# Kernel optimization log

Hardware: AMD Instinct MI355X
Metric: run time of the kernel (lower is better)

## Reference

```python
import jax, jax.numpy as jnp
import numpy as np

IN_FEATS = 512
OUT_FEATS = 512
N = 8192
M = 8192


def setup_inputs() -> dict:
    key = jax.random.key(0)
    k1, k2, k3 = jax.random.split(key, 3)
    feat_p = jax.random.normal(k1, (N, IN_FEATS), dtype=jnp.float32)
    feat_s = jax.random.normal(k2, (M, IN_FEATS), dtype=jnp.float32)
    # He (kaiming uniform) init: bound = sqrt(6 / fan_in)
    bound = float(np.sqrt(6.0 / IN_FEATS))
    weight_a = jax.random.uniform(k3, (IN_FEATS, OUT_FEATS), dtype=jnp.float32,
                                  minval=-bound, maxval=bound)
    return {"feat_p": feat_p, "feat_s": feat_s, "weight_a": weight_a}


def reference(feat_p, feat_s, weight_a):
    h_i = feat_p @ weight_a            # [N, out]
    h_j = feat_s @ weight_a            # [M, out]
    a_ij = jax.nn.relu(h_i @ h_j.T)    # [N, M]
    fro = jnp.sqrt(jnp.sum(a_ij * a_ij))
    alpha = a_ij / fro                 # global Frobenius-norm normalization
    c_i = alpha @ feat_s               # [N, in]
    return c_i
```

## Files before the change

kernel.cpp:

```cpp
#include <hip/hip_runtime.h>
#include <hip/hip_bf16.h>

#define NROWS 8192
#define DIM   512

typedef short v8s __attribute__((ext_vector_type(8)));
typedef float v4f __attribute__((ext_vector_type(4)));

#define ASM_VMCNT(n) asm volatile("s_waitcnt vmcnt(" #n ")" ::: "memory")
#define ASM_LGKM0    asm volatile("s_waitcnt lgkmcnt(0)" ::: "memory")
#define ASM_FENCE    asm volatile("" ::: "memory")
#define BAR          __builtin_amdgcn_s_barrier()

__device__ __forceinline__ short f2bf(float f) {
    union { float f; unsigned u; } v; v.f = f;
    unsigned r = (v.u + 0x7fffu + ((v.u >> 16) & 1u)) >> 16;
    return (short)r;
}

__device__ __forceinline__ void stage16(const void* g, void* l) {
    typedef __attribute__((address_space(1))) const unsigned GA;
    typedef __attribute__((address_space(3))) unsigned LA;
    __builtin_amdgcn_global_load_lds((GA*)(const unsigned*)g, (LA*)(unsigned*)l, 16, 0, 0);
}

__global__ __launch_bounds__(256) void transpose_cast_kernel(
        const float* __restrict__ in, short* __restrict__ out, int R, int C) {
    __shared__ float t[32][33];
    const int lx = threadIdx.x & 31;
    const int ly = threadIdx.x >> 5;
    const int r0 = blockIdx.x * 32;
    const int c0 = blockIdx.y * 32;
#pragma unroll
    for (int p = 0; p < 4; ++p)
        t[ly + 8 * p][lx] = in[(size_t)(r0 + ly + 8 * p) * C + c0 + lx];
    __syncthreads();
#pragma unroll
    for (int p = 0; p < 4; ++p)
        out[(size_t)(c0 + ly + 8 * p) * R + r0 + lx] = f2bf(t[lx][ly + 8 * p]);
}

__global__ __launch_bounds__(512) void gemm1_kernel(
        const float* __restrict__ Fp, const float* __restrict__ Fs,
        const short* __restrict__ WT,
        short* __restrict__ Hp, short* __restrict__ Hs) {
    const float* F = blockIdx.z ? Fs : Fp;
    short* H = blockIdx.z ? Hs : Hp;
    const int lane = threadIdx.x & 63;
    const int wid  = threadIdx.x >> 6;
    const int lr = lane & 15, lg = lane >> 4;
    const int r0 = blockIdx.x * 128 + wid * 16;
    const int c0 = blockIdx.y * 256;

    v8s a[16];
#pragma unroll
    for (int kk = 0; kk < 16; ++kk) {
        const float* ap = F + (size_t)(r0 + lr) * DIM + kk * 32 + lg * 8;
        float4 f0 = *(const float4*)ap;
        float4 f1 = *(const float4*)(ap + 4);
        v8s t;
        t[0] = f2bf(f0.x); t[1] = f2bf(f0.y); t[2] = f2bf(f0.z); t[3] = f2bf(f0.w);
        t[4] = f2bf(f1.x); t[5] = f2bf(f1.y); t[6] = f2bf(f1.z); t[7] = f2bf(f1.w);
        a[kk] = t;
    }

    for (int ctp = 0; ctp < 8; ++ctp) {
        const int cb = c0 + ctp * 32;
        v4f acc0 = {}, acc1 = {};
#pragma unroll
        for (int kk = 0; kk < 16; ++kk) {
            v8s b0 = *(const v8s*)(WT + (size_t)(cb + lr) * DIM + kk * 32 + lg * 8);
            v8s b1 = *(const v8s*)(WT + (size_t)(cb + 16 + lr) * DIM + kk * 32 + lg * 8);
            acc0 = __builtin_amdgcn_mfma_f32_16x16x32_bf16(a[kk], b0, acc0, 0, 0, 0);
            acc1 = __builtin_amdgcn_mfma_f32_16x16x32_bf16(a[kk], b1, acc1, 0, 0, 0);
        }
#pragma unroll
        for (int i = 0; i < 4; ++i) {
            H[(size_t)(r0 + lg * 4 + i) * DIM + cb + lr]      = f2bf(acc0[i]);
            H[(size_t)(r0 + lg * 4 + i) * DIM + cb + 16 + lr] = f2bf(acc1[i]);
        }
    }
}

#define JSPLIT 2
#define JT_PER_BLOCK (NROWS / 64 / JSPLIT)

__device__ __forceinline__ void stage_full(const char* __restrict__ HsB,
        char* ringW, int j0, int tid) {
#pragma unroll
    for (int s = 0; s < 8; ++s) {
        const int L = s * 8192 + tid * 16;
        const int row = L >> 10;
        const int c = (L & 1023) ^ ((row & 7) << 4);
        stage16(HsB + ((size_t)(j0 + row) << 10) + c, ringW + L);
    }
}

__device__ __forceinline__ void phase_b(const short (*SbR)[72], const v8s* bF,
        v4f (&accC)[16], int lr, int lg) {
    __builtin_amdgcn_s_setprio(1);
#pragma unroll
    for (int kc2 = 0; kc2 < 2; ++kc2)
#pragma unroll
        for (int mt = 0; mt < 4; ++mt) {
            v8s aS = *(const v8s*)&SbR[mt * 16 + lr][kc2 * 32 + lg * 8];
#pragma unroll
            for (int ct = 0; ct < 4; ++ct)
                accC[mt * 4 + ct] = __builtin_amdgcn_mfma_f32_16x16x32_bf16(
                    aS, bF[ct * 2 + kc2], accC[mt * 4 + ct], 0, 0, 0);
        }
    __builtin_amdgcn_s_setprio(0);
}

__global__ __launch_bounds__(512, 2) void fused_kernel(
        const short* __restrict__ Hp, const short* __restrict__ Hs,
        const short* __restrict__ FsT, float* __restrict__ Cacc,
        float* __restrict__ ssq) {
    __shared__ __align__(16) short HsL[2][64][512];
    __shared__ __align__(16) short Sb[2][64][72];

    const int tid  = threadIdx.x;
    const int lane = tid & 63;
    const int wid  = tid >> 6;
    const int lr = lane & 15, lg = lane >> 4;
    const int strip = wid >> 1;
    const int half  = wid & 1;

    const int nwg = gridDim.x * gridDim.y;
    const int bid = blockIdx.x + gridDim.x * blockIdx.y;
    const int cpx = nwg >> 3;
    const int swz = (bid & 7) * cpx + (bid >> 3);
    const int bx = swz % gridDim.x;
    const int by = swz / gridDim.x;

    const int m0  = bx * 64;
    const int jt0 = by * JT_PER_BLOCK;

    v8s afrag[16];
#pragma unroll
    for (int kk = 0; kk < 16; ++kk)
        afrag[kk] = *(const v8s*)(Hp +
            (size_t)(m0 + strip * 16 + lr) * DIM + kk * 32 + lg * 8);

    v4f accC[16] = {};
    v8s bF[8];
    float ssq_l = 0.f;

    stage_full((const char*)Hs, (char*)&HsL[0][0][0], jt0 * 64, tid);
    ASM_VMCNT(0);

    const int xo = (lr & 7) << 4;

    for (int t = 0; t < JT_PER_BLOCK; ++t) {
        const int jcur  = (jt0 + t) * 64;
        const int jnext = (t + 1 < JT_PER_BLOCK) ? jcur + 64 : jt0 * 64;
        const char* ringR = (const char*)&HsL[t & 1][0][0];
        char*       ringW = (char*)&HsL[(t + 1) & 1][0][0];

        BAR;
        ASM_FENCE;

        stage_full((const char*)Hs, ringW, jnext, tid);

        v4f s0 = {}, s1 = {};
        {
            const char* rp0 = ringR + (size_t)(half * 32 + lr) * 1024;
            const char* rp1 = rp0 + 16 * 1024;
            __builtin_amdgcn_s_setprio(1);
#pragma unroll
            for (int kk = 0; kk < 16; ++kk) {
                const int off = (kk * 64 + lg * 16) ^ xo;
                v8s hb0 = *(const v8s*)(rp0 + off);
                v8s hb1 = *(const v8s*)(rp1 + off);
                s0 = __builtin_amdgcn_mfma_f32_16x16x32_bf16(afrag[kk], hb0, s0, 0, 0, 0);
                s1 = __builtin_amdgcn_mfma_f32_16x16x32_bf16(afrag[kk], hb1, s1, 0, 0, 0);
            }
            __builtin_amdgcn_s_setprio(0);
        }

        short (*SbW)[72] = Sb[t & 1];
#pragma unroll
        for (int i = 0; i < 4; ++i) {
            float v0 = fmaxf(s0[i], 0.f), v1 = fmaxf(s1[i], 0.f);
            ssq_l += v0 * v0 + v1 * v1;
            const int r = strip * 16 + lg * 4 + i;
            SbW[r][(half * 2 + 0) * 16 + lr] = f2bf(v0);
            SbW[r][(half * 2 + 1) * 16 + lr] = f2bf(v1);
        }

        if (t > 0) {
            ASM_VMCNT(8);
            phase_b(Sb[(t - 1) & 1], bF, accC, lr, lg);
        }
        ASM_LGKM0;

        ASM_FENCE;
#pragma unroll
        for (int ct = 0; ct < 4; ++ct)
#pragma unroll
            for (int kc2 = 0; kc2 < 2; ++kc2)
                bF[ct * 2 + kc2] = *(const v8s*)(FsT +
                    (size_t)(wid * 64 + ct * 16 + lr) * NROWS + jcur + kc2 * 32 + lg * 8);
        ASM_VMCNT(8);
    }

    BAR;
    ASM_VMCNT(0);
    phase_b(Sb[(JT_PER_BLOCK - 1) & 1], bF, accC, lr, lg);

    float w = ssq_l;
#pragma unroll
    for (int off = 32; off; off >>= 1) w += __shfl_down(w, off);
    if (lane == 0) atomicAdd(ssq, w);

#pragma unroll
    for (int mt = 0; mt < 4; ++mt)
#pragma unroll
        for (int ct = 0; ct < 4; ++ct)
#pragma unroll
            for (int i = 0; i < 4; ++i)
                atomicAdd(&Cacc[(size_t)(m0 + mt * 16 + lg * 4 + i) * DIM +
                                wid * 64 + ct * 16 + lr],
                          accC[mt * 4 + ct][i]);
}

__global__ __launch_bounds__(256) void scale_kernel(float* __restrict__ C,
                                                    const float* __restrict__ ssq) {
    const float rs = 1.0f / sqrtf(*ssq);
    const size_t i = (size_t)blockIdx.x * blockDim.x + threadIdx.x;
    float4* p = (float4*)C;
    float4 v = p[i];
    v.x *= rs; v.y *= rs; v.z *= rs; v.w *= rs;
    p[i] = v;
}

extern "C" void kernel_launch(void* const* d_in, const int* in_sizes, int n_in,
                              void* d_out, int out_size, void* d_ws, size_t ws_size,
                              hipStream_t stream) {
    const float* feat_p   = (const float*)d_in[0];
    const float* feat_s   = (const float*)d_in[1];
    const float* weight_a = (const float*)d_in[2];

    char* ws = (char*)d_ws;
    float* ssqp = (float*)ws;
    short* WT   = (short*)(ws + 512);
    short* Hp   = (short*)(ws + 512 + 524288);
    short* Hs   = (short*)(ws + 512 + 524288 + 8388608);
    short* FsT  = (short*)(ws + 512 + 524288 + 16777216);

    transpose_cast_kernel<<<dim3(DIM / 32, DIM / 32), 256, 0, stream>>>(weight_a, WT, DIM, DIM);
    transpose_cast_kernel<<<dim3(NROWS / 32, DIM / 32), 256, 0, stream>>>(feat_s, FsT, NROWS, DIM);

    gemm1_kernel<<<dim3(NROWS / 128, 2, 2), 512, 0, stream>>>(
        feat_p, feat_s, WT, Hp, Hs);

    hipMemsetAsync(d_out, 0, (size_t)out_size * sizeof(float), stream);
    hipMemsetAsync(ssqp, 0, sizeof(float), stream);

    fused_kernel<<<dim3(NROWS / 64, JSPLIT), 512, 0, stream>>>(Hp, Hs, FsT, (float*)d_out, ssqp);

    scale_kernel<<<(out_size / 4 + 255) / 256, 256, 0, stream>>>((float*)d_out, ssqp);
}
```

Baseline: 353.0 us.

## Peel first tile and interleave phase-B MFMAs into second half of score GEMM

Peels the first j-tile out of the main loop and, in steady-state iterations, interleaves the previous tile's alpha@feat_s MFMAs with the second half of the current tile's score MFMAs. The goal is a denser mix of independent MFMA chains and LDS reads, so the dependent s0/s1 accumulation chains and the separate phase_b block no longer serialize. Phase B now runs before the ReLU/store of the current tile rather than after it. This adds code size and register pressure, and it moves the vmcnt wait earlier.

```diff
diff --git a/kernel.cpp b/kernel.cpp
--- a/kernel.cpp
+++ b/kernel.cpp
@@ -96,6 +96,16 @@
     }
 }
 
+__device__ __forceinline__ void load_bF(v8s (&bF)[8], const short* __restrict__ FsT,
+        int j, int wid, int lr, int lg) {
+#pragma unroll
+    for (int ct = 0; ct < 4; ++ct)
+#pragma unroll
+        for (int kc2 = 0; kc2 < 2; ++kc2)
+            bF[ct * 2 + kc2] = *(const v8s*)(FsT +
+                (size_t)(wid * 64 + ct * 16 + lr) * NROWS + j + kc2 * 32 + lg * 8);
+}
+
 __device__ __forceinline__ void phase_b(const short (*SbR)[72], const v8s* bF,
         v4f (&accC)[16], int lr, int lg) {
     __builtin_amdgcn_s_setprio(1);
@@ -150,35 +160,31 @@
     ASM_VMCNT(0);
 
     const int xo = (lr & 7) << 4;
-
-    for (int t = 0; t < JT_PER_BLOCK; ++t) {
-        const int jcur  = (jt0 + t) * 64;
-        const int jnext = (t + 1 < JT_PER_BLOCK) ? jcur + 64 : jt0 * 64;
-        const char* ringR = (const char*)&HsL[t & 1][0][0];
-        char*       ringW = (char*)&HsL[(t + 1) & 1][0][0];
-
-        BAR;
-        ASM_FENCE;
-
-        stage_full((const char*)Hs, ringW, jnext, tid);
+    const char* rbase0;
+    {
+    }
+
+    {
+        const char* ringR = (const char*)&HsL[0][0][0];
+        char*       ringW = (char*)&HsL[1][0][0];
+        BAR; ASM_FENCE;
+        stage_full((const char*)Hs, ringW, (jt0 + 1) * 64, tid);
 
         v4f s0 = {}, s1 = {};
-        {
-            const char* rp0 = ringR + (size_t)(half * 32 + lr) * 1024;
-            const char* rp1 = rp0 + 16 * 1024;
-            __builtin_amdgcn_s_setprio(1);
-#pragma unroll
-            for (int kk = 0; kk < 16; ++kk) {
-                const int off = (kk * 64 + lg * 16) ^ xo;
-                v8s hb0 = *(const v8s*)(rp0 + off);
-                v8s hb1 = *(const v8s*)(rp1 + off);
-                s0 = __builtin_amdgcn_mfma_f32_16x16x32_bf16(afrag[kk], hb0, s0, 0, 0, 0);
-                s1 = __builtin_amdgcn_mfma_f32_16x16x32_bf16(afrag[kk], hb1, s1, 0, 0, 0);
-            }
-            __builtin_amdgcn_s_setprio(0);
-        }
-
-        short (*SbW)[72] = Sb[t & 1];
+        const char* rp0 = ringR + (size_t)(half * 32 + lr) * 1024;
+        const char* rp1 = rp0 + 16 * 1024;
+        __builtin_amdgcn_s_setprio(1);
+#pragma unroll
+        for (int kk = 0; kk < 16; ++kk) {
+            const int off = (kk * 64 + lg * 16) ^ xo;
+            v8s hb0 = *(const v8s*)(rp0 + off);
+            v8s hb1 = *(const v8s*)(rp1 + off);
+            s0 = __builtin_amdgcn_mfma_f32_16x16x32_bf16(afrag[kk], hb0, s0, 0, 0, 0);
+            s1 = __builtin_amdgcn_mfma_f32_16x16x32_bf16(afrag[kk], hb1, s1, 0, 0, 0);
+        }
+        __builtin_amdgcn_s_setprio(0);
+
+        short (*SbW)[72] = Sb[0];
 #pragma unroll
         for (int i = 0; i < 4; ++i) {
             float v0 = fmaxf(s0[i], 0.f), v1 = fmaxf(s1[i], 0.f);
@@ -187,20 +193,69 @@
             SbW[r][(half * 2 + 0) * 16 + lr] = f2bf(v0);
             SbW[r][(half * 2 + 1) * 16 + lr] = f2bf(v1);
         }
-
-        if (t > 0) {
-            ASM_VMCNT(8);
-            phase_b(Sb[(t - 1) & 1], bF, accC, lr, lg);
-        }
         ASM_LGKM0;
-
         ASM_FENCE;
-#pragma unroll
-        for (int ct = 0; ct < 4; ++ct)
-#pragma unroll
-            for (int kc2 = 0; kc2 < 2; ++kc2)
-                bF[ct * 2 + kc2] = *(const v8s*)(FsT +
-                    (size_t)(wid * 64 + ct * 16 + lr) * NROWS + jcur + kc2 * 32 + lg * 8);
+        load_bF(bF, FsT, jt0 * 64, wid, lr, lg);
+        ASM_VMCNT(8);
+    }
+
+    for (int t = 1; t < JT_PER_BLOCK; ++t) {
+        const int jcur  = (jt0 + t) * 64;
+        const int jnext = (t + 1 < JT_PER_BLOCK) ? jcur + 64 : jt0 * 64;
+        const char* ringR = (const char*)&HsL[t & 1][0][0];
+        char*       ringW = (char*)&HsL[(t + 1) & 1][0][0];
+        const short (*SbR)[72] = Sb[(t & 1) ^ 1];
+
+        BAR; ASM_FENCE;
+        stage_full((const char*)Hs, ringW, jnext, tid);
+
+        v4f s0 = {}, s1 = {};
+        const char* rp0 = ringR + (size_t)(half * 32 + lr) * 1024;
+        const char* rp1 = rp0 + 16 * 1024;
+        __builtin_amdgcn_s_setprio(1);
+
+#pragma unroll
+        for (int kk = 0; kk < 8; ++kk) {
+            const int off = (kk * 64 + lg * 16) ^ xo;
+            v8s hb0 = *(const v8s*)(rp0 + off);
+            v8s hb1 = *(const v8s*)(rp1 + off);
+            s0 = __builtin_amdgcn_mfma_f32_16x16x32_bf16(afrag[kk], hb0, s0, 0, 0, 0);
+            s1 = __builtin_amdgcn_mfma_f32_16x16x32_bf16(afrag[kk], hb1, s1, 0, 0, 0);
+        }
+
+        ASM_VMCNT(8);
+
+#pragma unroll
+        for (int g = 0; g < 8; ++g) {
+            const int kk = 8 + g;
+            const int off = (kk * 64 + lg * 16) ^ xo;
+            v8s hb0 = *(const v8s*)(rp0 + off);
+            v8s hb1 = *(const v8s*)(rp1 + off);
+            s0 = __builtin_amdgcn_mfma_f32_16x16x32_bf16(afrag[kk], hb0, s0, 0, 0, 0);
+            s1 = __builtin_amdgcn_mfma_f32_16x16x32_bf16(afrag[kk], hb1, s1, 0, 0, 0);
+
+            const int mt = g & 3, kc2 = g >> 2;
+            v8s aS = *(const v8s*)&SbR[mt * 16 + lr][kc2 * 32 + lg * 8];
+#pragma unroll
+            for (int ct = 0; ct < 4; ++ct)
+                accC[mt * 4 + ct] = __builtin_amdgcn_mfma_f32_16x16x32_bf16(
+                    aS, bF[ct * 2 + kc2], accC[mt * 4 + ct], 0, 0, 0);
+        }
+        __builtin_amdgcn_s_setprio(0);
+
+        short (*SbW)[72] = Sb[t & 1];
+#pragma unroll
+        for (int i = 0; i < 4; ++i) {
+            float v0 = fmaxf(s0[i], 0.f), v1 = fmaxf(s1[i], 0.f);
+            ssq_l += v0 * v0 + v1 * v1;
+            const int r = strip * 16 + lg * 4 + i;
+            SbW[r][(half * 2 + 0) * 16 + lr] = f2bf(v0);
+            SbW[r][(half * 2 + 1) * 16 + lr] = f2bf(v1);
+        }
+        ASM_LGKM0;
+
+        ASM_FENCE;
+        load_bF(bF, FsT, jcur, wid, lr, lg);
         ASM_VMCNT(8);
     }
 
```

Result: no change. 351.2 us (-0.5%).

## Use 32x32x16 MFMA with split-K across wave pairs for score tile

Applied to the files above, without the earlier changes.

Phase A now computes the 64x64 score tile with 32x32x16 bf16 MFMAs. Each wave covers a 32x32 sub-tile over half of the K dimension, and the two partial sums are exchanged through a new LDS buffer, then reduced before ReLU and the bf16 cast. The larger MFMA shape is meant to cut LDS fragment loads and instruction count per FLOP. In exchange it adds an LDS partial-sum exchange and two extra block barriers per iteration. The Sb buffer is no longer double-buffered, which adds synchronization.

```diff
diff --git a/kernel.cpp b/kernel.cpp
--- a/kernel.cpp
+++ b/kernel.cpp
@@ -6,6 +6,7 @@
 
 typedef short v8s __attribute__((ext_vector_type(8)));
 typedef float v4f __attribute__((ext_vector_type(4)));
+typedef float v16f __attribute__((ext_vector_type(16)));
 
 #define ASM_VMCNT(n) asm volatile("s_waitcnt vmcnt(" #n ")" ::: "memory")
 #define ASM_LGKM0    asm volatile("s_waitcnt lgkmcnt(0)" ::: "memory")
@@ -96,6 +97,16 @@
     }
 }
 
+__device__ __forceinline__ void load_bF(v8s (&bF)[8], const short* __restrict__ FsT,
+        int j, int wid, int lr, int lg) {
+#pragma unroll
+    for (int ct = 0; ct < 4; ++ct)
+#pragma unroll
+        for (int kc2 = 0; kc2 < 2; ++kc2)
+            bF[ct * 2 + kc2] = *(const v8s*)(FsT +
+                (size_t)(wid * 64 + ct * 16 + lr) * NROWS + j + kc2 * 32 + lg * 8);
+}
+
 __device__ __forceinline__ void phase_b(const short (*SbR)[72], const v8s* bF,
         v4f (&accC)[16], int lr, int lg) {
     __builtin_amdgcn_s_setprio(1);
@@ -117,14 +128,17 @@
         const short* __restrict__ FsT, float* __restrict__ Cacc,
         float* __restrict__ ssq) {
     __shared__ __align__(16) short HsL[2][64][512];
-    __shared__ __align__(16) short Sb[2][64][72];
+    __shared__ __align__(16) short Sb[64][72];
+    __shared__ __align__(16) float Pb[8][64][8];
 
     const int tid  = threadIdx.x;
     const int lane = tid & 63;
     const int wid  = tid >> 6;
     const int lr = lane & 15, lg = lane >> 4;
-    const int strip = wid >> 1;
-    const int half  = wid & 1;
+    const int l31 = lane & 31, l5 = lane >> 5;
+    const int kh = wid & 1;
+    const int jh = (wid >> 1) & 1;
+    const int mh = wid >> 2;
 
     const int nwg = gridDim.x * gridDim.y;
     const int bid = blockIdx.x + gridDim.x * blockIdx.y;
@@ -138,9 +152,9 @@
 
     v8s afrag[16];
 #pragma unroll
-    for (int kk = 0; kk < 16; ++kk)
-        afrag[kk] = *(const v8s*)(Hp +
-            (size_t)(m0 + strip * 16 + lr) * DIM + kk * 32 + lg * 8);
+    for (int kc = 0; kc < 16; ++kc)
+        afrag[kc] = *(const v8s*)(Hp +
+            (size_t)(m0 + mh * 32 + l31) * DIM + kh * 256 + kc * 16 + l5 * 8);
 
     v4f accC[16] = {};
     v8s bF[8];
@@ -149,7 +163,8 @@
     stage_full((const char*)Hs, (char*)&HsL[0][0][0], jt0 * 64, tid);
     ASM_VMCNT(0);
 
-    const int xo = (lr & 7) << 4;
+    const int xo2 = (l31 & 7) << 4;
+    const int colbase = kh * 512 + l5 * 16;
 
     for (int t = 0; t < JT_PER_BLOCK; ++t) {
         const int jcur  = (jt0 + t) * 64;
@@ -159,54 +174,87 @@
 
         BAR;
         ASM_FENCE;
-
         stage_full((const char*)Hs, ringW, jnext, tid);
 
-        v4f s0 = {}, s1 = {};
+        v16f pacc = {};
         {
-            const char* rp0 = ringR + (size_t)(half * 32 + lr) * 1024;
-            const char* rp1 = rp0 + 16 * 1024;
+            const char* rb = ringR + (size_t)(jh * 32 + l31) * 1024;
             __builtin_amdgcn_s_setprio(1);
 #pragma unroll
-            for (int kk = 0; kk < 16; ++kk) {
-                const int off = (kk * 64 + lg * 16) ^ xo;
-                v8s hb0 = *(const v8s*)(rp0 + off);
-                v8s hb1 = *(const v8s*)(rp1 + off);
-                s0 = __builtin_amdgcn_mfma_f32_16x16x32_bf16(afrag[kk], hb0, s0, 0, 0, 0);
-                s1 = __builtin_amdgcn_mfma_f32_16x16x32_bf16(afrag[kk], hb1, s1, 0, 0, 0);
+            for (int kc = 0; kc < 16; ++kc) {
+                v8s hb = *(const v8s*)(rb + ((colbase + kc * 32) ^ xo2));
+                pacc = __builtin_amdgcn_mfma_f32_32x32x16_bf16(afrag[kc], hb, pacc, 0, 0, 0);
             }
             __builtin_amdgcn_s_setprio(0);
         }
 
-        short (*SbW)[72] = Sb[t & 1];
-#pragma unroll
-        for (int i = 0; i < 4; ++i) {
-            float v0 = fmaxf(s0[i], 0.f), v1 = fmaxf(s1[i], 0.f);
-            ssq_l += v0 * v0 + v1 * v1;
-            const int r = strip * 16 + lg * 4 + i;
-            SbW[r][(half * 2 + 0) * 16 + lr] = f2bf(v0);
-            SbW[r][(half * 2 + 1) * 16 + lr] = f2bf(v1);
+        {
+            float* gp = &Pb[wid][lane][0];
+            if (kh == 0) {
+                v4f g0 = {pacc[8], pacc[9], pacc[10], pacc[11]};
+                v4f g1 = {pacc[12], pacc[13], pacc[14], pacc[15]};
+                *(v4f*)gp = g0; *(v4f*)(gp + 4) = g1;
+            } else {
+                v4f g0 = {pacc[0], pacc[1], pacc[2], pacc[3]};
+                v4f g1 = {pacc[4], pacc[5], pacc[6], pacc[7]};
+                *(v4f*)gp = g0; *(v4f*)(gp + 4) = g1;
+            }
+        }
+        ASM_LGKM0; BAR;
+
+        short sb16[8];
+        {
+            const float* pp = &Pb[wid ^ 1][lane][0];
+            v4f q0 = *(const v4f*)pp;
+            v4f q1 = *(const v4f*)(pp + 4);
+            float sv[8];
+            if (kh == 0) {
+                sv[0] = pacc[0] + q0[0]; sv[1] = pacc[1] + q0[1];
+                sv[2] = pacc[2] + q0[2]; sv[3] = pacc[3] + q0[3];
+                sv[4] = pacc[4] + q1[0]; sv[5] = pacc[5] + q1[1];
+                sv[6] = pacc[6] + q1[2]; sv[7] = pacc[7] + q1[3];
+            } else {
+                sv[0] = pacc[8]  + q0[0]; sv[1] = pacc[9]  + q0[1];
+                sv[2] = pacc[10] + q0[2]; sv[3] = pacc[11] + q0[3];
+                sv[4] = pacc[12] + q1[0]; sv[5] = pacc[13] + q1[1];
+                sv[6] = pacc[14] + q1[2]; sv[7] = pacc[15] + q1[3];
+            }
+#pragma unroll
+            for (int e = 0; e < 8; ++e) {
+                float v = fmaxf(sv[e], 0.f);
+                ssq_l += v * v;
+                sb16[e] = f2bf(v);
+            }
         }
 
         if (t > 0) {
             ASM_VMCNT(8);
-            phase_b(Sb[(t - 1) & 1], bF, accC, lr, lg);
-        }
+            phase_b(Sb, bF, accC, lr, lg);
+        }
+        ASM_LGKM0; BAR;
+
+        {
+            const int cb = jh * 32 + l31;
+            if (kh == 0) {
+#pragma unroll
+                for (int e = 0; e < 8; ++e)
+                    Sb[mh * 32 + (e & 3) + 8 * (e >> 2) + 4 * l5][cb] = sb16[e];
+            } else {
+#pragma unroll
+                for (int e = 0; e < 8; ++e)
+                    Sb[mh * 32 + 16 + (e & 3) + 8 * (e >> 2) + 4 * l5][cb] = sb16[e];
+            }
+        }
+
+        ASM_FENCE;
+        load_bF(bF, FsT, jcur, wid, lr, lg);
         ASM_LGKM0;
-
-        ASM_FENCE;
-#pragma unroll
-        for (int ct = 0; ct < 4; ++ct)
-#pragma unroll
-            for (int kc2 = 0; kc2 < 2; ++kc2)
-                bF[ct * 2 + kc2] = *(const v8s*)(FsT +
-                    (size_t)(wid * 64 + ct * 16 + lr) * NROWS + jcur + kc2 * 32 + lg * 8);
         ASM_VMCNT(8);
     }
 
     BAR;
     ASM_VMCNT(0);
-    phase_b(Sb[(JT_PER_BLOCK - 1) & 1], bF, accC, lr, lg);
+    phase_b(Sb, bF, accC, lr, lg);
 
     float w = ssq_l;
 #pragma unroll
```

Result: slower. 432.4 us (+22.5%).

## Double M tile per block to 128 rows and drop Sb double-buffered software pipeline

Applied to the files above, without the earlier changes.

Each block now covers 128 query rows, one 16-row strip per wave, instead of 64 rows, and the J range is split four ways. This halves how often each staged Hs tile and each FsT fragment is fetched per output row. The one-iteration-delayed phase-B pipeline with a double-buffered Sb is replaced by a single Sb buffer, a barrier, and an immediate second GEMM each iteration. Loading bF at the top of the iteration and waiting on vmcnt(0) at the end adds serialization. Accumulator registers double to 32 v4f, which adds register pressure at 2 blocks per CU.

```diff
diff --git a/kernel.cpp b/kernel.cpp
--- a/kernel.cpp
+++ b/kernel.cpp
@@ -82,7 +82,8 @@
     }
 }
 
-#define JSPLIT 2
+#define MTILE  128
+#define JSPLIT 4
 #define JT_PER_BLOCK (NROWS / 64 / JSPLIT)
 
 __device__ __forceinline__ void stage_full(const char* __restrict__ HsB,
@@ -96,20 +97,14 @@
     }
 }
 
-__device__ __forceinline__ void phase_b(const short (*SbR)[72], const v8s* bF,
-        v4f (&accC)[16], int lr, int lg) {
-    __builtin_amdgcn_s_setprio(1);
-#pragma unroll
-    for (int kc2 = 0; kc2 < 2; ++kc2)
-#pragma unroll
-        for (int mt = 0; mt < 4; ++mt) {
-            v8s aS = *(const v8s*)&SbR[mt * 16 + lr][kc2 * 32 + lg * 8];
-#pragma unroll
-            for (int ct = 0; ct < 4; ++ct)
-                accC[mt * 4 + ct] = __builtin_amdgcn_mfma_f32_16x16x32_bf16(
-                    aS, bF[ct * 2 + kc2], accC[mt * 4 + ct], 0, 0, 0);
-        }
-    __builtin_amdgcn_s_setprio(0);
+__device__ __forceinline__ void load_bF(v8s (&bF)[8], const short* __restrict__ FsT,
+        int j, int wid, int lr, int lg) {
+#pragma unroll
+    for (int ct = 0; ct < 4; ++ct)
+#pragma unroll
+        for (int kc2 = 0; kc2 < 2; ++kc2)
+            bF[ct * 2 + kc2] = *(const v8s*)(FsT +
+                (size_t)(wid * 64 + ct * 16 + lr) * NROWS + j + kc2 * 32 + lg * 8);
 }
 
 __global__ __launch_bounds__(512, 2) void fused_kernel(
@@ -117,14 +112,12 @@
         const short* __restrict__ FsT, float* __restrict__ Cacc,
         float* __restrict__ ssq) {
     __shared__ __align__(16) short HsL[2][64][512];
-    __shared__ __align__(16) short Sb[2][64][72];
+    __shared__ __align__(16) short Sb[128][72];
 
     const int tid  = threadIdx.x;
     const int lane = tid & 63;
     const int wid  = tid >> 6;
     const int lr = lane & 15, lg = lane >> 4;
-    const int strip = wid >> 1;
-    const int half  = wid & 1;
 
     const int nwg = gridDim.x * gridDim.y;
     const int bid = blockIdx.x + gridDim.x * blockIdx.y;
@@ -133,16 +126,16 @@
     const int bx = swz % gridDim.x;
     const int by = swz / gridDim.x;
 
-    const int m0  = bx * 64;
+    const int m0  = bx * MTILE;
     const int jt0 = by * JT_PER_BLOCK;
 
     v8s afrag[16];
 #pragma unroll
     for (int kk = 0; kk < 16; ++kk)
         afrag[kk] = *(const v8s*)(Hp +
-            (size_t)(m0 + strip * 16 + lr) * DIM + kk * 32 + lg * 8);
-
-    v4f accC[16] = {};
+            (size_t)(m0 + wid * 16 + lr) * DIM + kk * 32 + lg * 8);
+
+    v4f accC[32] = {};
     v8s bF[8];
     float ssq_l = 0.f;
 
@@ -160,53 +153,51 @@
         BAR;
         ASM_FENCE;
 
+        load_bF(bF, FsT, jcur, wid, lr, lg);
+        ASM_FENCE;
         stage_full((const char*)Hs, ringW, jnext, tid);
 
-        v4f s0 = {}, s1 = {};
+        v4f s[4] = {};
         {
-            const char* rp0 = ringR + (size_t)(half * 32 + lr) * 1024;
-            const char* rp1 = rp0 + 16 * 1024;
             __builtin_amdgcn_s_setprio(1);
 #pragma unroll
             for (int kk = 0; kk < 16; ++kk) {
                 const int off = (kk * 64 + lg * 16) ^ xo;
-                v8s hb0 = *(const v8s*)(rp0 + off);
-                v8s hb1 = *(const v8s*)(rp1 + off);
-                s0 = __builtin_amdgcn_mfma_f32_16x16x32_bf16(afrag[kk], hb0, s0, 0, 0, 0);
-                s1 = __builtin_amdgcn_mfma_f32_16x16x32_bf16(afrag[kk], hb1, s1, 0, 0, 0);
+#pragma unroll
+                for (int ct = 0; ct < 4; ++ct) {
+                    v8s hb = *(const v8s*)(ringR + (size_t)(ct * 16 + lr) * 1024 + off);
+                    s[ct] = __builtin_amdgcn_mfma_f32_16x16x32_bf16(afrag[kk], hb, s[ct], 0, 0, 0);
+                }
             }
             __builtin_amdgcn_s_setprio(0);
         }
 
-        short (*SbW)[72] = Sb[t & 1];
-#pragma unroll
-        for (int i = 0; i < 4; ++i) {
-            float v0 = fmaxf(s0[i], 0.f), v1 = fmaxf(s1[i], 0.f);
-            ssq_l += v0 * v0 + v1 * v1;
-            const int r = strip * 16 + lg * 4 + i;
-            SbW[r][(half * 2 + 0) * 16 + lr] = f2bf(v0);
-            SbW[r][(half * 2 + 1) * 16 + lr] = f2bf(v1);
-        }
-
-        if (t > 0) {
-            ASM_VMCNT(8);
-            phase_b(Sb[(t - 1) & 1], bF, accC, lr, lg);
-        }
-        ASM_LGKM0;
-
-        ASM_FENCE;
 #pragma unroll
         for (int ct = 0; ct < 4; ++ct)
 #pragma unroll
-            for (int kc2 = 0; kc2 < 2; ++kc2)
-                bF[ct * 2 + kc2] = *(const v8s*)(FsT +
-                    (size_t)(wid * 64 + ct * 16 + lr) * NROWS + jcur + kc2 * 32 + lg * 8);
+            for (int i = 0; i < 4; ++i) {
+                float v = fmaxf(s[ct][i], 0.f);
+                ssq_l += v * v;
+                Sb[wid * 16 + lg * 4 + i][ct * 16 + lr] = f2bf(v);
+            }
+        ASM_LGKM0; BAR;
+
         ASM_VMCNT(8);
-    }
-
-    BAR;
-    ASM_VMCNT(0);
-    phase_b(Sb[(JT_PER_BLOCK - 1) & 1], bF, accC, lr, lg);
+        __builtin_amdgcn_s_setprio(1);
+#pragma unroll
+        for (int kc2 = 0; kc2 < 2; ++kc2)
+#pragma unroll
+            for (int mt = 0; mt < 8; ++mt) {
+                v8s aS = *(const v8s*)&Sb[mt * 16 + lr][kc2 * 32 + lg * 8];
+#pragma unroll
+                for (int ct = 0; ct < 4; ++ct)
+                    accC[mt * 4 + ct] = __builtin_amdgcn_mfma_f32_16x16x32_bf16(
+                        aS, bF[ct * 2 + kc2], accC[mt * 4 + ct], 0, 0, 0);
+            }
+        __builtin_amdgcn_s_setprio(0);
+
+        ASM_VMCNT(0);
+    }
 
     float w = ssq_l;
 #pragma unroll
@@ -214,7 +205,7 @@
     if (lane == 0) atomicAdd(ssq, w);
 
 #pragma unroll
-    for (int mt = 0; mt < 4; ++mt)
+    for (int mt = 0; mt < 8; ++mt)
 #pragma unroll
         for (int ct = 0; ct < 4; ++ct)
 #pragma unroll
@@ -257,7 +248,8 @@
     hipMemsetAsync(d_out, 0, (size_t)out_size * sizeof(float), stream);
     hipMemsetAsync(ssqp, 0, sizeof(float), stream);
 
-    fused_kernel<<<dim3(NROWS / 64, JSPLIT), 512, 0, stream>>>(Hp, Hs, FsT, (float*)d_out, ssqp);
+    fused_kernel<<<dim3(NROWS / MTILE, JSPLIT), 512, 0, stream>>>(
+        Hp, Hs, FsT, (float*)d_out, ssqp);
 
     scale_kernel<<<(out_size / 4 + 255) / 256, 256, 0, stream>>>((float*)d_out, ssqp);
 }
```

After: 392.8 us. 1.11x slower.
